# Kernel tuning notes

Hardware: AMD Instinct MI355X
Metric: run time of the kernel (lower is better)

## Reference

```python
import jax, jax.numpy as jnp
import numpy as np
import math

HIDDEN = 768
NUM_HEADS = 12
HEAD_DIM = HIDDEN // NUM_HEADS
EPS = 1e-05
MU_LEARNED = 0.0    # registered buffer init value (inference mode)
SIGMA_LEARNED = 1.0 # registered buffer init value (inference mode)
SCALES = (0.5, 1.0, 2.0)


def make_pe(n, d):
    # Sinusoidal positional encoding, identical to PositionalEncoding buffer.
    pos = np.arange(n, dtype=np.float32)[:, None]
    div = np.exp(np.arange(0, d, 2, dtype=np.float32) * (-math.log(10000.0) / d))
    pe = np.zeros((n, d), dtype=np.float32)
    pe[:, 0::2] = np.sin(pos * div)
    pe[:, 1::2] = np.cos(pos * div)
    return jnp.asarray(pe)


def setup_inputs() -> dict:
    key = jax.random.key(0)
    ks = jax.random.split(key, 12)
    B, C, Hh, Ww = 8, 256, 32, 32
    feat = jax.random.normal(ks[0], (B, C, Hh, Ww), jnp.float32)
    I = jax.random.uniform(ks[1], (B, 1, Hh, Ww), jnp.float32)
    sc_c = 1.0 / math.sqrt(C)
    sd = 1.0 / math.sqrt(HIDDEN)
    proj_w = jax.random.normal(ks[2], (C, HIDDEN), jnp.float32) * sc_c  # 1x1 conv as matmul
    proj_b = jnp.zeros((HIDDEN,), jnp.float32)
    wq = jax.random.normal(ks[3], (HIDDEN, HIDDEN), jnp.float32) * sd
    bq = jnp.zeros((HIDDEN,), jnp.float32)
    wk = jax.random.normal(ks[4], (HIDDEN, HIDDEN), jnp.float32) * sd
    bk = jnp.zeros((HIDDEN,), jnp.float32)
    wv = jax.random.normal(ks[5], (HIDDEN, HIDDEN), jnp.float32) * sd
    bv = jnp.zeros((HIDDEN,), jnp.float32)
    wo = jax.random.normal(ks[6], (HIDDEN, HIDDEN), jnp.float32) * sd
    bo = jnp.zeros((HIDDEN,), jnp.float32)
    lam = jnp.float32(0.5)
    return dict(feat=feat, I=I, proj_w=proj_w, proj_b=proj_b,
                wq=wq, bq=bq, wk=wk, bk=bk, wv=wv, bv=bv, wo=wo, bo=bo, lam=lam)


def reference(feat, I, proj_w, proj_b, wq, bq, wk, bk, wv, bv, wo, bo, lam):
    B, C, Hh, Ww = feat.shape
    N = Hh * Ww
    # HiddenFeatureProjection: 1x1 conv projection -> flatten -> tokens [B, N, D]
    tokens = jnp.einsum('bchw,cd->bhwd', feat, proj_w).reshape(B, N, HIDDEN) + proj_b
    tokens = tokens + make_pe(N, HIDDEN)[None]
    # GaussianWeightModule (inference path, learned buffers mu=0, sigma=1)
    G = sum(jnp.exp(-(I - MU_LEARNED) ** 2 / (2.0 * (k * SIGMA_LEARNED) ** 2 + EPS))
            for k in SCALES) / float(len(SCALES))  # [B,1,H,W]
    g = G.reshape(B, N)                              # H*W == N by construction
    bias = g[:, :, None] * g[:, None, :]             # [B, N, N] outer product
    # GaussianEnhancedAttention
    q = (tokens @ wq + bq).reshape(B, N, NUM_HEADS, HEAD_DIM).transpose(0, 2, 1, 3)
    k = (tokens @ wk + bk).reshape(B, N, NUM_HEADS, HEAD_DIM).transpose(0, 2, 1, 3)
    v = (tokens @ wv + bv).reshape(B, N, NUM_HEADS, HEAD_DIM).transpose(0, 2, 1, 3)
    scores = jnp.einsum('bhnd,bhmd->bhnm', q, k) / math.sqrt(HEAD_DIM)
    scores = scores + lam * bias[:, None, :, :]
    attn = jax.nn.softmax(scores, axis=-1)
    out = jnp.einsum('bhnm,bhmd->bhnd', attn, v).transpose(0, 2, 1, 3).reshape(B, N, HIDDEN)
    return out @ wo + bo
```

## Files before the change

kernel.cpp:

```cpp
#include <hip/hip_runtime.h>
#include <hip/hip_bf16.h>
#include <math.h>

#define HIDDEN 768
#define NHEADS 12
#define HDIM   64
#define NTOK   1024
#define BATCH  8
#define CIN    256
#define M_ALL  (BATCH * NTOK)
#define LSTR   72

typedef __hip_bfloat16 bf16;
typedef short frag8 __attribute__((ext_vector_type(8)));
typedef short s16x4 __attribute__((ext_vector_type(4)));
typedef float f32x4 __attribute__((ext_vector_type(4)));

#define GL2LDS(gp, lp) \
    __builtin_amdgcn_global_load_lds((const __attribute__((address_space(1))) void*)(gp), \
                                     (__attribute__((address_space(3))) void*)(lp), 16, 0, 0)

__device__ __forceinline__ short f2bs(float x){
    union { bf16 h; short s; } u; u.h = __float2bfloat16(x); return u.s;
}

__device__ __forceinline__ float gaussw(float x){
    float x2 = x * x;
    return (__expf(-x2 / 0.50001f) + __expf(-x2 / 2.00001f) + __expf(-x2 / 8.00001f)) * (1.0f / 3.0f);
}

__global__ __launch_bounds__(256) void prep_all(
    const float* __restrict__ wq, const float* __restrict__ wk,
    const float* __restrict__ wv, const float* __restrict__ wo,
    const float* __restrict__ proj_w, const float* __restrict__ feat,
    short* __restrict__ wtqkv, short* __restrict__ wtp, short* __restrict__ featT)
{
    __shared__ short t[64][65];
    const int blk = blockIdx.x;
    const float* W; short* WT; int K, N, k0, n0;
    if (blk < 576) {
        int p = blk / 144, rem = blk % 144;
        const float* srcs[4] = {wq, wk, wv, wo};
        W = srcs[p]; WT = wtqkv + (size_t)p * HIDDEN * HIDDEN;
        K = HIDDEN; N = HIDDEN; k0 = (rem / 12) * 64; n0 = (rem % 12) * 64;
    } else if (blk < 624) {
        int rem = blk - 576;
        W = proj_w; WT = wtp;
        K = CIN; N = HIDDEN; k0 = (rem / 12) * 64; n0 = (rem % 12) * 64;
    } else {
        int rem = blk - 624;
        int b = rem / 64; rem %= 64;
        W = feat + (size_t)b * CIN * NTOK; WT = featT + (size_t)b * NTOK * CIN;
        K = CIN; N = NTOK; k0 = (rem / 16) * 64; n0 = (rem % 16) * 64;
    }
    const int tid = threadIdx.x;
    #pragma unroll
    for (int it = 0; it < 16; it++) {
        int e = tid + 256 * it;
        int kk = e / 64, nn = e % 64;
        t[kk][nn] = f2bs(W[(size_t)(k0 + kk) * N + n0 + nn]);
    }
    __syncthreads();
    #pragma unroll
    for (int it = 0; it < 16; it++) {
        int e = tid + 256 * it;
        int nn = e / 64, kk = e % 64;
        WT[(size_t)(n0 + nn) * K + k0 + kk] = t[kk][nn];
    }
}

__global__ __launch_bounds__(256) void transpose_v(
    const short* __restrict__ v, short* __restrict__ vT,
    const float* __restrict__ I, float* __restrict__ g)
{
    if (blockIdx.y == BATCH * NHEADS) {
        int idx = blockIdx.x * 512 + threadIdx.x * 2;
        g[idx]     = gaussw(I[idx]);
        g[idx + 1] = gaussw(I[idx + 1]);
        return;
    }
    __shared__ short t[64][65];
    const int nt = blockIdx.x;
    const int bh = blockIdx.y;
    const int b = bh / NHEADS, h = bh % NHEADS;
    const int tid = threadIdx.x;
    #pragma unroll
    for (int it = 0; it < 16; it++) {
        int e = tid + 256 * it;
        int rr = e / 64, cc = e % 64;
        t[rr][cc] = v[(size_t)(b * NTOK + nt * 64 + rr) * HIDDEN + h * HDIM + cc];
    }
    __syncthreads();
    #pragma unroll
    for (int it = 0; it < 16; it++) {
        int e = tid + 256 * it;
        int c2 = e / 64, r2 = e % 64;
        vT[((size_t)bh * HDIM + c2) * NTOK + nt * 64 + r2] = t[r2][c2];
    }
}

__global__ __launch_bounds__(256) void gemm_mfma128(
    const short* __restrict__ A, const short* __restrict__ WT0, long wt_z,
    const float* __restrict__ b0, const float* __restrict__ b1, const float* __restrict__ b2,
    short* o0, short* o1, short* o2, int K)
{
    __shared__ short Al[128 * 32];
    __shared__ short Bl[128 * 32];
    const int z = blockIdx.z;
    const short* WT  = WT0 + (size_t)z * wt_z;
    const float* bias = (z == 0) ? b0 : (z == 1) ? b1 : b2;
    short* outv       = (z == 0) ? o0 : (z == 1) ? o1 : o2;

    const int tid  = threadIdx.x;
    const int m0   = blockIdx.x * 128;
    const int n0   = blockIdx.y * 128;
    const int lane = tid & 63, wid = tid >> 6;
    const int wm   = (wid >> 1) * 64, wn = (wid & 1) * 64;
    const int l16  = lane & 15, quad = lane >> 4;

    const int sr  = lane >> 2;
    const int ssg = (lane & 3) ^ ((sr >> 1) & 3);
    const int fsw = (l16 >> 1) & 3;

    const f32x4 z4 = {0.f, 0.f, 0.f, 0.f};
    f32x4 acc[4][4];
    #pragma unroll
    for (int i = 0; i < 4; i++)
        #pragma unroll
        for (int j = 0; j < 4; j++) acc[i][j] = z4;

    for (int k0 = 0; k0 < K; k0 += 32) {
        #pragma unroll
        for (int t = 0; t < 2; t++) {
            int rbase = wid * 32 + t * 16;
            int r = rbase + sr;
            GL2LDS(A  + (size_t)(m0 + r) * K + k0 + ssg * 8, &Al[rbase * 32]);
            GL2LDS(WT + (size_t)(n0 + r) * K + k0 + ssg * 8, &Bl[rbase * 32]);
        }
        __syncthreads();
        frag8 af[4], bfr[4];
        #pragma unroll
        for (int i = 0; i < 4; i++)
            af[i]  = *(const frag8*)&Al[(wm + i * 16 + l16) * 32 + ((quad ^ fsw) * 8)];
        #pragma unroll
        for (int j = 0; j < 4; j++)
            bfr[j] = *(const frag8*)&Bl[(wn + j * 16 + l16) * 32 + ((quad ^ fsw) * 8)];
        #pragma unroll
        for (int i = 0; i < 4; i++)
            #pragma unroll
            for (int j = 0; j < 4; j++)
                acc[i][j] = __builtin_amdgcn_mfma_f32_16x16x32_bf16(af[i], bfr[j], acc[i][j], 0, 0, 0);
        __syncthreads();
    }

    #pragma unroll
    for (int i = 0; i < 4; i++) {
        #pragma unroll
        for (int r = 0; r < 4; r++) {
            int m = m0 + wm + i * 16 + quad * 4 + r;
            #pragma unroll
            for (int j = 0; j < 4; j++) {
                int col = n0 + wn + j * 16 + l16;
                outv[(size_t)m * HIDDEN + col] = f2bs(acc[i][j][r] + bias[col]);
            }
        }
    }
}

template<int MODE>
__global__ __launch_bounds__(256) void gemm_mfma64(
    const short* __restrict__ A, const short* __restrict__ WT,
    const float* __restrict__ bias, void* outv, int K)
{
    __shared__ short Al[64 * 32];
    __shared__ short Bl[128 * 32];
    const int tid  = threadIdx.x;
    const int m0   = blockIdx.x * 64;
    const int n0   = blockIdx.y * 128;
    const int lane = tid & 63, wid = tid >> 6;
    const int wn   = wid * 32;
    const int l16  = lane & 15, quad = lane >> 4;

    const int sr  = lane >> 2;
    const int ssg = (lane & 3) ^ ((sr >> 1) & 3);
    const int fsw = (l16 >> 1) & 3;

    const f32x4 z4 = {0.f, 0.f, 0.f, 0.f};
    f32x4 acc[4][2];
    #pragma unroll
    for (int i = 0; i < 4; i++)
        #pragma unroll
        for (int j = 0; j < 2; j++) acc[i][j] = z4;

    for (int k0 = 0; k0 < K; k0 += 32) {
        GL2LDS(A + (size_t)(m0 + wid * 16 + sr) * K + k0 + ssg * 8, &Al[(wid * 16) * 32]);
        #pragma unroll
        for (int t = 0; t < 2; t++) {
            int rbase = wid * 32 + t * 16;
            GL2LDS(WT + (size_t)(n0 + rbase + sr) * K + k0 + ssg * 8, &Bl[rbase * 32]);
        }
        __syncthreads();
        frag8 af[4], bfr[2];
        #pragma unroll
        for (int i = 0; i < 4; i++)
            af[i]  = *(const frag8*)&Al[(i * 16 + l16) * 32 + ((quad ^ fsw) * 8)];
        #pragma unroll
        for (int j = 0; j < 2; j++)
            bfr[j] = *(const frag8*)&Bl[(wn + j * 16 + l16) * 32 + ((quad ^ fsw) * 8)];
        #pragma unroll
        for (int i = 0; i < 4; i++)
            #pragma unroll
            for (int j = 0; j < 2; j++)
                acc[i][j] = __builtin_amdgcn_mfma_f32_16x16x32_bf16(af[i], bfr[j], acc[i][j], 0, 0, 0);
        __syncthreads();
    }

    const float kfac = -9.210340371976184f / 768.0f;
    #pragma unroll
    for (int i = 0; i < 4; i++) {
        #pragma unroll
        for (int r = 0; r < 4; r++) {
            int m = m0 + i * 16 + quad * 4 + r;
            #pragma unroll
            for (int j = 0; j < 2; j++) {
                int col = n0 + wn + j * 16 + l16;
                float val = acc[i][j][r] + bias[col];
                if (MODE == 1) {
                    int n_tok = m & (NTOK - 1);
                    float ang = (float)n_tok * expf((float)(2 * (col >> 1)) * kfac);
                    val += (col & 1) ? cosf(ang) : sinf(ang);
                }
                if (MODE == 2) ((float*)outv)[(size_t)m * HIDDEN + col] = val;
                else           ((short*)outv)[(size_t)m * HIDDEN + col] = f2bs(val);
            }
        }
    }
}

__global__ __launch_bounds__(256, 3) void attn_mfma(
    const short* __restrict__ q, const short* __restrict__ k, const short* __restrict__ vT,
    const float* __restrict__ g, const float* __restrict__ lam_p, short* __restrict__ out)
{
    __shared__ short Pl[128 * LSTR];
    __shared__ short Ks[2][64 * 64];
    __shared__ short Vt[2][64 * 64];

    const int tid  = threadIdx.x;
    const int lin  = blockIdx.x;
    const int xcd  = lin & 7, slot = lin >> 3;
    const int b    = xcd;
    const int h    = slot >> 3;
    const int qt   = slot & 7;
    const float L2E  = 1.4426950408889634f;
    const float lam2 = lam_p[0] * L2E;
    const float scl  = 0.125f * L2E;
    const int lane = tid & 63, wave = tid >> 6;
    const int l16  = lane & 15, quad = lane >> 4;

    const int sr   = lane >> 3;
    const int slin = lane & 7;
    const int ssg  = slin ^ sr;
    const int fsw  = l16 & 7;

    const size_t kb  = (size_t)b * NTOK * HIDDEN + h * HDIM;
    const size_t vtb = (size_t)(b * NHEADS + h) * HDIM * NTOK;
    const float* gk  = g + b * NTOK;

    frag8 aq[2][2];
    #pragma unroll
    for (int half = 0; half < 2; half++)
        #pragma unroll
        for (int kc = 0; kc < 2; kc++)
            aq[half][kc] = *(const frag8*)&q[(size_t)(b * NTOK + qt * 128 + wave * 32 + half * 16 + l16) * HIDDEN
                                             + h * HDIM + kc * 32 + quad * 8];
    float gq[2];
    #pragma unroll
    for (int half = 0; half < 2; half++)
        gq[half] = lam2 * gk[qt * 128 + wave * 32 + half * 16 + l16];

    #pragma unroll
    for (int t = 0; t < 2; t++) {
        int rbase = wave * 16 + t * 8;
        int r = rbase + sr;
        GL2LDS(k  + kb  + (size_t)r * HIDDEN + ssg * 8,  &Ks[0][rbase * 64]);
        GL2LDS(vT + vtb + (size_t)r * NTOK + ssg * 8,    &Vt[0][rbase * 64]);
    }
    __syncthreads();

    const f32x4 z4 = {0.f, 0.f, 0.f, 0.f};
    f32x4 o_acc[2][4];
    #pragma unroll
    for (int half = 0; half < 2; half++)
        #pragma unroll
        for (int d = 0; d < 4; d++) o_acc[half][d] = z4;
    float l_run[2] = {0.f, 0.f};

    for (int jt = 0; jt < 16; jt++) {
        const int cur = jt & 1;
        if (jt < 15) {
            #pragma unroll
            for (int t = 0; t < 2; t++) {
                int rbase = wave * 16 + t * 8;
                int r = rbase + sr;
                GL2LDS(k  + kb  + (size_t)((jt + 1) * 64 + r) * HIDDEN + ssg * 8, &Ks[cur ^ 1][rbase * 64]);
                GL2LDS(vT + vtb + (size_t)r * NTOK + (jt + 1) * 64 + ssg * 8,     &Vt[cur ^ 1][rbase * 64]);
            }
        }
        f32x4 gk4[4];
        #pragma unroll
        for (int t4 = 0; t4 < 4; t4++)
            gk4[t4] = *(const f32x4*)&gk[jt * 64 + t4 * 16 + quad * 4];

        float p[2][4][4];
        #pragma unroll
        for (int t4 = 0; t4 < 4; t4++) {
            frag8 ak0 = *(const frag8*)&Ks[cur][(t4 * 16 + l16) * 64 + ((quad ^ fsw) * 8)];
            frag8 ak1 = *(const frag8*)&Ks[cur][(t4 * 16 + l16) * 64 + (((quad + 4) ^ fsw) * 8)];
            #pragma unroll
            for (int half = 0; half < 2; half++) {
                f32x4 a = z4;
                a = __builtin_amdgcn_mfma_f32_16x16x32_bf16(ak0, aq[half][0], a, 0, 0, 0);
                a = __builtin_amdgcn_mfma_f32_16x16x32_bf16(ak1, aq[half][1], a, 0, 0, 0);
                #pragma unroll
                for (int r = 0; r < 4; r++) p[half][t4][r] = a[r];
            }
        }

        #pragma unroll
        for (int half = 0; half < 2; half++)
            #pragma unroll
            for (int t4 = 0; t4 < 4; t4++) {
                s16x4 w;
                #pragma unroll
                for (int r = 0; r < 4; r++) {
                    float e = exp2f(p[half][t4][r] * scl + gq[half] * gk4[t4][r]);
                    l_run[half] += e;
                    w[r] = f2bs(e);
                }
                *(s16x4*)&Pl[(wave * 32 + half * 16 + l16) * LSTR + t4 * 16 + quad * 4] = w;
            }

        frag8 ap[2][2];
        #pragma unroll
        for (int half = 0; half < 2; half++)
            #pragma unroll
            for (int kc = 0; kc < 2; kc++)
                ap[half][kc] = *(const frag8*)&Pl[(wave * 32 + half * 16 + l16) * LSTR + kc * 32 + quad * 8];
        #pragma unroll
        for (int d = 0; d < 4; d++) {
            frag8 av0 = *(const frag8*)&Vt[cur][(d * 16 + l16) * 64 + ((quad ^ fsw) * 8)];
            frag8 av1 = *(const frag8*)&Vt[cur][(d * 16 + l16) * 64 + (((quad + 4) ^ fsw) * 8)];
            #pragma unroll
            for (int half = 0; half < 2; half++) {
                o_acc[half][d] = __builtin_amdgcn_mfma_f32_16x16x32_bf16(ap[half][0], av0, o_acc[half][d], 0, 0, 0);
                o_acc[half][d] = __builtin_amdgcn_mfma_f32_16x16x32_bf16(ap[half][1], av1, o_acc[half][d], 0, 0, 0);
            }
        }
        __syncthreads();
    }

    #pragma unroll
    for (int half = 0; half < 2; half++) {
        float l = l_run[half];
        l += __shfl_xor(l, 16);
        l += __shfl_xor(l, 32);
        #pragma unroll
        for (int r = 0; r < 4; r++) {
            float lq = __shfl(l, (lane & 48) | (quad * 4 + r));
            float inv_l = 1.0f / lq;
            int row = qt * 128 + wave * 32 + half * 16 + quad * 4 + r;
            #pragma unroll
            for (int d = 0; d < 4; d++)
                out[(size_t)(b * NTOK + row) * HIDDEN + h * HDIM + d * 16 + l16]
                    = f2bs(o_acc[half][d][r] * inv_l);
        }
    }
}

extern "C" void kernel_launch(void* const* d_in, const int* in_sizes, int n_in,
                              void* d_out, int out_size, void* d_ws, size_t ws_size,
                              hipStream_t stream)
{
    const float* feat   = (const float*)d_in[0];
    const float* I      = (const float*)d_in[1];
    const float* proj_w = (const float*)d_in[2];
    const float* proj_b = (const float*)d_in[3];
    const float* wq     = (const float*)d_in[4];
    const float* bq     = (const float*)d_in[5];
    const float* wk     = (const float*)d_in[6];
    const float* bk     = (const float*)d_in[7];
    const float* wv     = (const float*)d_in[8];
    const float* bv     = (const float*)d_in[9];
    const float* wo     = (const float*)d_in[10];
    const float* bo     = (const float*)d_in[11];
    const float* lam    = (const float*)d_in[12];
    float* out = (float*)d_out;

    short* wtqkv = (short*)d_ws;
    short* wto   = wtqkv + (size_t)3 * HIDDEN * HIDDEN;
    short* wtp   = wto   + (size_t)HIDDEN * HIDDEN;
    short* tokens= wtp   + (size_t)HIDDEN * CIN;
    short* qbuf  = tokens+ (size_t)M_ALL * HIDDEN;
    short* featT = qbuf;
    short* vTb   = tokens;
    short* kbuf  = (short*)d_out;
    short* vbuf  = kbuf + (size_t)M_ALL * HIDDEN;
    float* gbuf  = (float*)wtp;

    prep_all<<<1136, 256, 0, stream>>>(wq, wk, wv, wo, proj_w, feat, wtqkv, wtp, featT);
    gemm_mfma64<1><<<dim3(128, 6), 256, 0, stream>>>(featT, wtp, proj_b, tokens, CIN);
    gemm_mfma128<<<dim3(64, 6, 3), 256, 0, stream>>>(tokens, wtqkv, (long)HIDDEN * HIDDEN,
                                                     bq, bk, bv,
                                                     qbuf, kbuf, vbuf, HIDDEN);
    transpose_v<<<dim3(16, 97), 256, 0, stream>>>(vbuf, vTb, I, gbuf);
    attn_mfma<<<768, 256, 0, stream>>>(qbuf, kbuf, vTb, gbuf, lam, qbuf);
    gemm_mfma64<2><<<dim3(128, 6), 256, 0, stream>>>(qbuf, wto, bo, out, HIDDEN);
}
```

Measured before the change: 237.7 us.

## Load K/V attention fragments directly from global instead of LDS double buffer

The attention kernel drops the double-buffered LDS staging of K and V tiles and their per-tile barriers. Each wave now loads its MFMA fragments straight from global memory (through cache), while the Gaussian weight vector is staged once into LDS. It also raises launch bounds to 4 blocks per CU and adds s_setprio around the MFMA sections. The goal is to remove LDS traffic and barriers and gain occupancy, at the cost of every wave issuing its own global loads of the same K/V data with no prefetch overlap.

```diff
diff --git a/kernel.cpp b/kernel.cpp
--- a/kernel.cpp
+++ b/kernel.cpp
@@ -237,13 +237,12 @@
     }
 }
 
-__global__ __launch_bounds__(256, 3) void attn_mfma(
+__global__ __launch_bounds__(256, 4) void attn_mfma(
     const short* __restrict__ q, const short* __restrict__ k, const short* __restrict__ vT,
     const float* __restrict__ g, const float* __restrict__ lam_p, short* __restrict__ out)
 {
     __shared__ short Pl[128 * LSTR];
-    __shared__ short Ks[2][64 * 64];
-    __shared__ short Vt[2][64 * 64];
+    __shared__ float gLs[NTOK];
 
     const int tid  = threadIdx.x;
     const int lin  = blockIdx.x;
@@ -257,14 +256,10 @@
     const int lane = tid & 63, wave = tid >> 6;
     const int l16  = lane & 15, quad = lane >> 4;
 
-    const int sr   = lane >> 3;
-    const int slin = lane & 7;
-    const int ssg  = slin ^ sr;
-    const int fsw  = l16 & 7;
-
     const size_t kb  = (size_t)b * NTOK * HIDDEN + h * HDIM;
     const size_t vtb = (size_t)(b * NHEADS + h) * HDIM * NTOK;
-    const float* gk  = g + b * NTOK;
+
+    for (int i = tid; i < NTOK; i += 256) gLs[i] = g[b * NTOK + i];
 
     frag8 aq[2][2];
     #pragma unroll
@@ -273,19 +268,12 @@
         for (int kc = 0; kc < 2; kc++)
             aq[half][kc] = *(const frag8*)&q[(size_t)(b * NTOK + qt * 128 + wave * 32 + half * 16 + l16) * HIDDEN
                                              + h * HDIM + kc * 32 + quad * 8];
+    __syncthreads();
+
     float gq[2];
     #pragma unroll
     for (int half = 0; half < 2; half++)
-        gq[half] = lam2 * gk[qt * 128 + wave * 32 + half * 16 + l16];
-
-    #pragma unroll
-    for (int t = 0; t < 2; t++) {
-        int rbase = wave * 16 + t * 8;
-        int r = rbase + sr;
-        GL2LDS(k  + kb  + (size_t)r * HIDDEN + ssg * 8,  &Ks[0][rbase * 64]);
-        GL2LDS(vT + vtb + (size_t)r * NTOK + ssg * 8,    &Vt[0][rbase * 64]);
-    }
-    __syncthreads();
+        gq[half] = lam2 * gLs[qt * 128 + wave * 32 + half * 16 + l16];
 
     const f32x4 z4 = {0.f, 0.f, 0.f, 0.f};
     f32x4 o_acc[2][4];
@@ -296,35 +284,42 @@
     float l_run[2] = {0.f, 0.f};
 
     for (int jt = 0; jt < 16; jt++) {
-        const int cur = jt & 1;
-        if (jt < 15) {
-            #pragma unroll
-            for (int t = 0; t < 2; t++) {
-                int rbase = wave * 16 + t * 8;
-                int r = rbase + sr;
-                GL2LDS(k  + kb  + (size_t)((jt + 1) * 64 + r) * HIDDEN + ssg * 8, &Ks[cur ^ 1][rbase * 64]);
-                GL2LDS(vT + vtb + (size_t)r * NTOK + (jt + 1) * 64 + ssg * 8,     &Vt[cur ^ 1][rbase * 64]);
-            }
-        }
-        f32x4 gk4[4];
-        #pragma unroll
-        for (int t4 = 0; t4 < 4; t4++)
-            gk4[t4] = *(const f32x4*)&gk[jt * 64 + t4 * 16 + quad * 4];
+        const short* kt = k + kb + (size_t)(jt * 64) * HIDDEN;
+        const short* vt = vT + vtb + jt * 64;
+
+        frag8 ak[4][2];
+        #pragma unroll
+        for (int t4 = 0; t4 < 4; t4++) {
+            ak[t4][0] = *(const frag8*)&kt[(size_t)(t4 * 16 + l16) * HIDDEN + quad * 8];
+            ak[t4][1] = *(const frag8*)&kt[(size_t)(t4 * 16 + l16) * HIDDEN + 32 + quad * 8];
+        }
 
         float p[2][4][4];
+        __builtin_amdgcn_s_setprio(1);
         #pragma unroll
         for (int t4 = 0; t4 < 4; t4++) {
-            frag8 ak0 = *(const frag8*)&Ks[cur][(t4 * 16 + l16) * 64 + ((quad ^ fsw) * 8)];
-            frag8 ak1 = *(const frag8*)&Ks[cur][(t4 * 16 + l16) * 64 + (((quad + 4) ^ fsw) * 8)];
             #pragma unroll
             for (int half = 0; half < 2; half++) {
                 f32x4 a = z4;
-                a = __builtin_amdgcn_mfma_f32_16x16x32_bf16(ak0, aq[half][0], a, 0, 0, 0);
-                a = __builtin_amdgcn_mfma_f32_16x16x32_bf16(ak1, aq[half][1], a, 0, 0, 0);
+                a = __builtin_amdgcn_mfma_f32_16x16x32_bf16(ak[t4][0], aq[half][0], a, 0, 0, 0);
+                a = __builtin_amdgcn_mfma_f32_16x16x32_bf16(ak[t4][1], aq[half][1], a, 0, 0, 0);
                 #pragma unroll
                 for (int r = 0; r < 4; r++) p[half][t4][r] = a[r];
             }
         }
+        __builtin_amdgcn_s_setprio(0);
+
+        frag8 av[4][2];
+        #pragma unroll
+        for (int d = 0; d < 4; d++) {
+            av[d][0] = *(const frag8*)&vt[(size_t)(d * 16 + l16) * NTOK + quad * 8];
+            av[d][1] = *(const frag8*)&vt[(size_t)(d * 16 + l16) * NTOK + 32 + quad * 8];
+        }
+
+        f32x4 gk4[4];
+        #pragma unroll
+        for (int t4 = 0; t4 < 4; t4++)
+            gk4[t4] = *(const f32x4*)&gLs[jt * 64 + t4 * 16 + quad * 4];
 
         #pragma unroll
         for (int half = 0; half < 2; half++)
@@ -346,17 +341,16 @@
             #pragma unroll
             for (int kc = 0; kc < 2; kc++)
                 ap[half][kc] = *(const frag8*)&Pl[(wave * 32 + half * 16 + l16) * LSTR + kc * 32 + quad * 8];
+        __builtin_amdgcn_s_setprio(1);
         #pragma unroll
         for (int d = 0; d < 4; d++) {
-            frag8 av0 = *(const frag8*)&Vt[cur][(d * 16 + l16) * 64 + ((quad ^ fsw) * 8)];
-            frag8 av1 = *(const frag8*)&Vt[cur][(d * 16 + l16) * 64 + (((quad + 4) ^ fsw) * 8)];
             #pragma unroll
             for (int half = 0; half < 2; half++) {
-                o_acc[half][d] = __builtin_amdgcn_mfma_f32_16x16x32_bf16(ap[half][0], av0, o_acc[half][d], 0, 0, 0);
-                o_acc[half][d] = __builtin_amdgcn_mfma_f32_16x16x32_bf16(ap[half][1], av1, o_acc[half][d], 0, 0, 0);
+                o_acc[half][d] = __builtin_amdgcn_mfma_f32_16x16x32_bf16(ap[half][0], av[d][0], o_acc[half][d], 0, 0, 0);
+                o_acc[half][d] = __builtin_amdgcn_mfma_f32_16x16x32_bf16(ap[half][1], av[d][1], o_acc[half][d], 0, 0, 0);
             }
         }
-        __syncthreads();
+        __builtin_amdgcn_s_setprio(0);
     }
 
     #pragma unroll
```

After: 341.7 us. 43.7% more time.
